# Performance work log

Measured on AMD Instinct MI355X. Metric: run time of the kernel, lower is better.

The kernel has to match this reference:

```python
import jax, jax.numpy as jnp
import numpy as np

N_HEADS = 8
D_K = 256
SCALE = D_K ** -0.5


def setup_inputs() -> dict:
    key = jax.random.key(0)
    k1, k2, k3 = jax.random.split(key, 3)
    B, C, H, W = 8, 256, 32, 32
    x = jax.random.normal(k1, (B, C, H, W), dtype=jnp.float32)
    Wp = jax.random.normal(k2, (C, N_HEADS * D_K * 3), dtype=jnp.float32) * (C ** -0.5)
    bp = jnp.zeros((N_HEADS * D_K * 3,), dtype=jnp.float32)
    Wo = jax.random.normal(k3, (N_HEADS * D_K, C), dtype=jnp.float32) * ((N_HEADS * D_K) ** -0.5)
    bo = jnp.zeros((C,), dtype=jnp.float32)
    return {"x": x, "Wp": Wp, "bp": bp, "Wo": Wo, "bo": bo}


def reference(x, Wp, bp, Wo, bo):
    B, C, H, W = x.shape
    S = H * W
    # [B,C,H,W] -> [B,S,C] tokens
    xt = x.reshape(B, C, S).transpose(0, 2, 1)
    qkv = (xt @ Wp + bp).reshape(B, S, N_HEADS, 3 * D_K)
    q, k, v = jnp.split(qkv, 3, axis=-1)  # each [B,S,H,dk]
    attn = jnp.einsum('bihd,bjhd->bijh', q, k) * SCALE
    attn = jax.nn.softmax(attn, axis=2)  # over j (keys)
    res = jnp.einsum('bijh,bjhd->bihd', attn, v).reshape(B, S, N_HEADS * D_K)
    res = res @ Wo + bo + xt  # residual
    return res.transpose(0, 2, 1).reshape(B, C, H, W)
```

## Files before the change

kernel.cpp:

```cpp
#include <hip/hip_runtime.h>

#define NH    8
#define DK    256
#define SS    1024
#define QSCALE 0.09016844136947155f

using frag8  = __attribute__((ext_vector_type(8))) short;
using f32x4  = __attribute__((ext_vector_type(4))) float;
using f32x16 = __attribute__((ext_vector_type(16))) float;

__device__ __forceinline__ unsigned short f2bf(float f) {
    unsigned int u = __float_as_uint(f);
    return (unsigned short)((u + 0x7FFFu + ((u >> 16) & 1u)) >> 16);
}

__device__ __forceinline__ void load_lds16(const void* g, void* l) {
    __builtin_amdgcn_global_load_lds(
        (const __attribute__((address_space(1))) unsigned int*)g,
        (__attribute__((address_space(3))) unsigned int*)l, 16, 0, 0);
}

__global__ __launch_bounds__(256) void k0_t(const float* __restrict__ in,
                                            unsigned short* __restrict__ out,
                                            int R, int C)
{
    __shared__ float tile[32][33];
    const int bz = blockIdx.z;
    const int c0 = blockIdx.x * 32, r0 = blockIdx.y * 32;
    const int tx = threadIdx.x & 31, ty = threadIdx.x >> 5;
    const float* ip = in + (size_t)bz * R * C;
    unsigned short* op = out + (size_t)bz * R * C;
#pragma unroll
    for (int j = 0; j < 4; j++)
        tile[ty + j * 8][tx] = ip[(size_t)(r0 + ty + j * 8) * C + c0 + tx];
    __syncthreads();
#pragma unroll
    for (int j = 0; j < 4; j++)
        op[(size_t)(c0 + ty + j * 8) * R + r0 + tx] = f2bf(tile[tx][ty + j * 8]);
}

__global__ __launch_bounds__(256) void k1_qkv(
    const unsigned short* __restrict__ xb, const unsigned short* __restrict__ Wpt,
    const float* __restrict__ bp,
    unsigned short* __restrict__ qb, unsigned short* __restrict__ kb,
    unsigned short* __restrict__ vb)
{
    __shared__ unsigned short As[128 * 32];
    __shared__ unsigned short Bs[128 * 32];
    const int t = threadIdx.x;
    const int wave = t >> 6, lane = t & 63;
    const int quad = lane >> 4, l16 = lane & 15;
    const int n0 = blockIdx.x * 128, m0 = blockIdx.y * 128;
    const int b = m0 >> 10, s0 = m0 & 1023;
    const int mq = (wave >> 1) * 64, nq = (wave & 1) * 64;
    const int lr = lane >> 2, lc = (lane & 3) * 8;

    const unsigned short* Ag = xb + (size_t)(b * 1024 + s0) * 256;
    const unsigned short* Bg = Wpt + (size_t)n0 * 256;

    f32x4 acc[4][4];
#pragma unroll
    for (int i = 0; i < 4; i++)
#pragma unroll
        for (int j = 0; j < 4; j++) acc[i][j] = (f32x4){0.f, 0.f, 0.f, 0.f};

    for (int k0 = 0; k0 < 256; k0 += 32) {
#pragma unroll
        for (int j = 0; j < 2; j++) {
            int ch = wave + j * 4;
            load_lds16(Ag + (size_t)(ch * 16 + lr) * 256 + k0 + lc, &As[ch * 512]);
            load_lds16(Bg + (size_t)(ch * 16 + lr) * 256 + k0 + lc, &Bs[ch * 512]);
        }
        __syncthreads();
        frag8 af[4], bf[4];
#pragma unroll
        for (int i = 0; i < 4; i++)
            af[i] = *(const frag8*)(&As[(mq + i * 16 + l16) * 32 + quad * 8]);
#pragma unroll
        for (int j = 0; j < 4; j++)
            bf[j] = *(const frag8*)(&Bs[(nq + j * 16 + l16) * 32 + quad * 8]);
#pragma unroll
        for (int i = 0; i < 4; i++)
#pragma unroll
            for (int j = 0; j < 4; j++)
                acc[i][j] = __builtin_amdgcn_mfma_f32_16x16x32_bf16(af[i], bf[j], acc[i][j], 0, 0, 0);
        __syncthreads();
    }

    const int h = n0 / 768;
    const int rem = n0 - h * 768;
    const int tt = rem >> 8;
    const int dbase = (rem & 255) + nq;
    const size_t bh = (size_t)(b * NH + h);
    float bias[4];
#pragma unroll
    for (int j = 0; j < 4; j++) bias[j] = bp[n0 + nq + j * 16 + l16];

    if (tt < 2) {
        const float sc = (tt == 0) ? QSCALE : 1.0f;
        unsigned short* dst = (tt == 0 ? qb : kb) + bh * SS * DK;
#pragma unroll
        for (int i = 0; i < 4; i++)
#pragma unroll
            for (int r = 0; r < 4; r++) {
                int s = s0 + mq + i * 16 + quad * 4 + r;
#pragma unroll
                for (int j = 0; j < 4; j++)
                    dst[(size_t)s * DK + dbase + j * 16 + l16] = f2bf((acc[i][j][r] + bias[j]) * sc);
            }
    } else {
        unsigned short* dst = vb + bh * DK * SS;
#pragma unroll
        for (int j = 0; j < 4; j++) {
            int d = dbase + j * 16 + l16;
#pragma unroll
            for (int i = 0; i < 4; i++)
#pragma unroll
                for (int r = 0; r < 4; r++)
                    dst[(size_t)d * SS + s0 + mq + i * 16 + quad * 4 + r]
                        = f2bf(acc[i][j][r] + bias[j]);
        }
    }
}

__global__ __launch_bounds__(256, 2) void k2_attn(
    const unsigned short* __restrict__ qb, const unsigned short* __restrict__ kb,
    const unsigned short* __restrict__ vb, unsigned short* __restrict__ ob)
{
    __shared__ unsigned short Ks[32 * 256];
    __shared__ unsigned short Vs[4 * 2048];
    __shared__ float Ls[4][32];

    const int t = threadIdx.x;
    const int wave = t >> 6, lane = t & 63;
    const int l32 = lane & 31, hw = lane >> 5;

    const int flat = blockIdx.x;
    const int xcd = flat & 7, tt2 = flat >> 3;
    const int qt = tt2 & 7;
    const int bh = xcd * 8 + (tt2 >> 3);

    const int qrow0 = qt * 128 + wave * 32;

    frag8 qf[16];
    {
        const unsigned short* qp = qb + ((size_t)bh * SS + qrow0 + l32) * DK + hw * 8;
#pragma unroll
        for (int s = 0; s < 16; s++) qf[s] = *(const frag8*)(qp + s * 16);
    }

    f32x16 acc[8];
#pragma unroll
    for (int nb = 0; nb < 8; nb++)
#pragma unroll
        for (int r = 0; r < 16; r++) acc[nb][r] = 0.f;
    float lsum = 0.f;

    const unsigned short* kstg = kb + ((size_t)bh * SS + (lane & 31)) * DK + (lane >> 5) * 8;
    const unsigned short* vstg = vb + (size_t)bh * DK * SS + (size_t)lane * SS;

    for (int kt = 0; kt < 32; kt++) {
#pragma unroll
        for (int jj = 0; jj < 4; jj++) {
            int i = wave * 4 + jj;
            load_lds16(kstg + (size_t)kt * 32 * DK + i * 16, &Ks[i * 512]);
            int kc = i & 3, dgrp = i >> 2;
            load_lds16(vstg + (size_t)dgrp * 64 * SS + kt * 32 + kc * 8,
                       &Vs[kc * 2048 + dgrp * 512]);
        }
        __syncthreads();

        f32x16 sa0, sa1;
#pragma unroll
        for (int r = 0; r < 16; r++) { sa0[r] = 0.f; sa1[r] = 0.f; }
#pragma unroll
        for (int s = 0; s < 16; s += 2) {
            frag8 kf0 = *(const frag8*)(&Ks[(2 * s + hw) * 256 + l32 * 8]);
            frag8 kf1 = *(const frag8*)(&Ks[(2 * s + 2 + hw) * 256 + l32 * 8]);
            sa0 = __builtin_amdgcn_mfma_f32_32x32x16_bf16(kf0, qf[s], sa0, 0, 0, 0);
            sa1 = __builtin_amdgcn_mfma_f32_32x32x16_bf16(kf1, qf[s + 1], sa1, 0, 0, 0);
        }

        frag8 pf[2];
#pragma unroll
        for (int half = 0; half < 2; half++) {
            float p[8], px[8];
#pragma unroll
            for (int e = 0; e < 8; e++) {
                p[e] = exp2f(sa0[half * 8 + e] + sa1[half * 8 + e]);
                lsum += p[e];
            }
#pragma unroll
            for (int e = 0; e < 8; e++) px[e] = __shfl_xor(p[e], 32);
            frag8 w;
#pragma unroll
            for (int j = 0; j < 4; j++) {
                w[j]     = (short)f2bf(hw ? px[4 + j] : p[j]);
                w[4 + j] = (short)f2bf(hw ? p[4 + j] : px[j]);
            }
            pf[half] = w;
        }

#pragma unroll
        for (int s01 = 0; s01 < 2; s01++)
#pragma unroll
            for (int nb = 0; nb < 8; nb++) {
                frag8 vf = *(const frag8*)(&Vs[(s01 * 2 + hw) * 2048 + (nb * 32 + l32) * 8]);
                acc[nb] = __builtin_amdgcn_mfma_f32_32x32x16_bf16(pf[s01], vf, acc[nb], 0, 0, 0);
            }
        __syncthreads();
    }

    lsum += __shfl_xor(lsum, 32);
    Ls[wave][l32] = 1.f / lsum;

    unsigned short* og = ob + ((size_t)bh * SS + qrow0) * DK + l32;
#pragma unroll
    for (int r = 0; r < 16; r++) {
        const int rowl = (r & 3) + 8 * (r >> 2) + 4 * hw;
        const float li = Ls[wave][rowl];
        unsigned short* orow = og + (size_t)rowl * DK;
#pragma unroll
        for (int nb = 0; nb < 8; nb++)
            orow[nb * 32] = f2bf(acc[nb][r] * li);
    }
}

__global__ __launch_bounds__(256) void k3_proj(
    const unsigned short* __restrict__ ob, const unsigned short* __restrict__ Wot,
    const float* __restrict__ bo, const float* __restrict__ x,
    float* __restrict__ out)
{
    __shared__ unsigned short As[64 * 32];
    __shared__ unsigned short Bs[64 * 32];
    const int t = threadIdx.x;
    const int wave = t >> 6, lane = t & 63;
    const int quad = lane >> 4, l16 = lane & 15;
    const int n0 = blockIdx.x * 64, m0 = blockIdx.y * 64;
    const int b = m0 >> 10, s0 = m0 & 1023;
    const int mq = (wave >> 1) * 32, nq = (wave & 1) * 32;
    const int lr = lane >> 2, lc = (lane & 3) * 8;

    const unsigned short* Bg = Wot + (size_t)n0 * 2048;

    f32x4 acc[2][2];
#pragma unroll
    for (int i = 0; i < 2; i++)
#pragma unroll
        for (int j = 0; j < 2; j++) acc[i][j] = (f32x4){0.f, 0.f, 0.f, 0.f};

    for (int k0 = 0; k0 < 2048; k0 += 32) {
        const int h = k0 >> 8, d0 = k0 & 255;
        const unsigned short* Ag = ob + (size_t)((b * 8 + h) * 1024 + s0) * 256 + d0;
        load_lds16(Ag + (size_t)(wave * 16 + lr) * 256 + lc, &As[wave * 512]);
        load_lds16(Bg + (size_t)(wave * 16 + lr) * 2048 + k0 + lc, &Bs[wave * 512]);
        __syncthreads();
        frag8 af[2], bf[2];
#pragma unroll
        for (int i = 0; i < 2; i++)
            af[i] = *(const frag8*)(&As[(mq + i * 16 + l16) * 32 + quad * 8]);
#pragma unroll
        for (int j = 0; j < 2; j++)
            bf[j] = *(const frag8*)(&Bs[(nq + j * 16 + l16) * 32 + quad * 8]);
#pragma unroll
        for (int i = 0; i < 2; i++)
#pragma unroll
            for (int j = 0; j < 2; j++)
                acc[i][j] = __builtin_amdgcn_mfma_f32_16x16x32_bf16(af[i], bf[j], acc[i][j], 0, 0, 0);
        __syncthreads();
    }

#pragma unroll
    for (int j = 0; j < 2; j++) {
        int c = n0 + nq + j * 16 + l16;
        float bias = bo[c];
#pragma unroll
        for (int i = 0; i < 2; i++) {
            int s = s0 + mq + i * 16 + quad * 4;
            size_t off = (size_t)(b * 256 + c) * 1024 + s;
            float4 xv = *(const float4*)(&x[off]);
            float4 ov;
            ov.x = acc[i][j][0] + bias + xv.x;
            ov.y = acc[i][j][1] + bias + xv.y;
            ov.z = acc[i][j][2] + bias + xv.z;
            ov.w = acc[i][j][3] + bias + xv.w;
            *(float4*)(&out[off]) = ov;
        }
    }
}

extern "C" void kernel_launch(void* const* d_in, const int* in_sizes, int n_in,
                              void* d_out, int out_size, void* d_ws, size_t ws_size,
                              hipStream_t stream)
{
    const float* x  = (const float*)d_in[0];
    const float* Wp = (const float*)d_in[1];
    const float* bp = (const float*)d_in[2];
    const float* Wo = (const float*)d_in[3];
    const float* bo = (const float*)d_in[4];
    float* out = (float*)d_out;

    char* ws = (char*)d_ws;
    unsigned short* qb  = (unsigned short*)(ws);
    unsigned short* kb  = (unsigned short*)(ws + 33554432);
    unsigned short* vb  = (unsigned short*)(ws + 67108864);
    unsigned short* xb  = (unsigned short*)(ws + 100663296);
    unsigned short* Wpt = (unsigned short*)(ws + 104857600);
    unsigned short* Wot = (unsigned short*)(ws + 108003328);

    k0_t<<<dim3(32, 8, 8), 256, 0, stream>>>(x, xb, 256, 1024);
    k0_t<<<dim3(192, 8, 1), 256, 0, stream>>>(Wp, Wpt, 256, 6144);
    k0_t<<<dim3(8, 64, 1), 256, 0, stream>>>(Wo, Wot, 2048, 256);
    k1_qkv<<<dim3(48, 64), 256, 0, stream>>>(xb, Wpt, bp, qb, kb, vb);
    k2_attn<<<dim3(512), 256, 0, stream>>>(qb, kb, vb, qb );
    k3_proj<<<dim3(4, 128), 256, 0, stream>>>(qb, Wot, bo, x, out);
}
```

Before: 257.8 us.

## Tile Q/K/V into LDS-contiguous layout and double-buffer K/V loads in attention

```diff
diff --git a/kernel.cpp b/kernel.cpp
--- a/kernel.cpp
+++ b/kernel.cpp
@@ -4,6 +4,7 @@
 #define DK    256
 #define SS    1024
 #define QSCALE 0.09016844136947155f
+#define TSH   8192
 
 using frag8  = __attribute__((ext_vector_type(8))) short;
 using f32x4  = __attribute__((ext_vector_type(4))) float;
@@ -19,6 +20,7 @@
         (const __attribute__((address_space(1))) unsigned int*)g,
         (__attribute__((address_space(3))) unsigned int*)l, 16, 0, 0);
 }
+
 
 __global__ __launch_bounds__(256) void k0_t(const float* __restrict__ in,
                                             unsigned short* __restrict__ out,
@@ -98,27 +100,32 @@
 
     if (tt < 2) {
         const float sc = (tt == 0) ? QSCALE : 1.0f;
-        unsigned short* dst = (tt == 0 ? qb : kb) + bh * SS * DK;
+        unsigned short* dst = (tt == 0 ? qb : kb) + bh * 32 * TSH;
 #pragma unroll
         for (int i = 0; i < 4; i++)
 #pragma unroll
             for (int r = 0; r < 4; r++) {
                 int s = s0 + mq + i * 16 + quad * 4 + r;
-#pragma unroll
-                for (int j = 0; j < 4; j++)
-                    dst[(size_t)s * DK + dbase + j * 16 + l16] = f2bf((acc[i][j][r] + bias[j]) * sc);
+                const size_t tb = (size_t)(s >> 5) * TSH + (s & 31) * 8;
+#pragma unroll
+                for (int j = 0; j < 4; j++) {
+                    int d = dbase + j * 16 + l16;
+                    dst[tb + (d >> 3) * 256 + (d & 7)] = f2bf((acc[i][j][r] + bias[j]) * sc);
+                }
             }
     } else {
-        unsigned short* dst = vb + bh * DK * SS;
+        unsigned short* dst = vb + bh * 32 * TSH;
 #pragma unroll
         for (int j = 0; j < 4; j++) {
             int d = dbase + j * 16 + l16;
 #pragma unroll
             for (int i = 0; i < 4; i++)
 #pragma unroll
-                for (int r = 0; r < 4; r++)
-                    dst[(size_t)d * SS + s0 + mq + i * 16 + quad * 4 + r]
+                for (int r = 0; r < 4; r++) {
+                    int s = s0 + mq + i * 16 + quad * 4 + r;
+                    dst[(size_t)(s >> 5) * TSH + ((s >> 3) & 3) * 2048 + d * 8 + (s & 7)]
                         = f2bf(acc[i][j][r] + bias[j]);
+                }
         }
     }
 }
@@ -127,9 +134,8 @@
     const unsigned short* __restrict__ qb, const unsigned short* __restrict__ kb,
     const unsigned short* __restrict__ vb, unsigned short* __restrict__ ob)
 {
-    __shared__ unsigned short Ks[32 * 256];
-    __shared__ unsigned short Vs[4 * 2048];
-    __shared__ float Ls[4][32];
+    __shared__ unsigned short Ks[2][TSH];
+    __shared__ unsigned short Vs[2][TSH];
 
     const int t = threadIdx.x;
     const int wave = t >> 6, lane = t & 63;
@@ -144,9 +150,10 @@
 
     frag8 qf[16];
     {
-        const unsigned short* qp = qb + ((size_t)bh * SS + qrow0 + l32) * DK + hw * 8;
-#pragma unroll
-        for (int s = 0; s < 16; s++) qf[s] = *(const frag8*)(qp + s * 16);
+        const unsigned short* qp = qb + ((size_t)bh * 32 + qt * 4 + wave) * TSH
+                                 + hw * 256 + l32 * 8;
+#pragma unroll
+        for (int s = 0; s < 16; s++) qf[s] = *(const frag8*)(qp + s * 512);
     }
 
     f32x16 acc[8];
@@ -156,27 +163,38 @@
         for (int r = 0; r < 16; r++) acc[nb][r] = 0.f;
     float lsum = 0.f;
 
-    const unsigned short* kstg = kb + ((size_t)bh * SS + (lane & 31)) * DK + (lane >> 5) * 8;
-    const unsigned short* vstg = vb + (size_t)bh * DK * SS + (size_t)lane * SS;
+    const unsigned short* kt0 = kb + (size_t)bh * 32 * TSH;
+    const unsigned short* vt0 = vb + (size_t)bh * 32 * TSH;
+
+#pragma unroll
+    for (int j = 0; j < 4; j++) {
+        int c = wave * 4 + j;
+        load_lds16(kt0 + c * 512 + lane * 8, &Ks[0][c * 512]);
+        load_lds16(vt0 + c * 512 + lane * 8, &Vs[0][c * 512]);
+    }
+    __syncthreads();
 
     for (int kt = 0; kt < 32; kt++) {
-#pragma unroll
-        for (int jj = 0; jj < 4; jj++) {
-            int i = wave * 4 + jj;
-            load_lds16(kstg + (size_t)kt * 32 * DK + i * 16, &Ks[i * 512]);
-            int kc = i & 3, dgrp = i >> 2;
-            load_lds16(vstg + (size_t)dgrp * 64 * SS + kt * 32 + kc * 8,
-                       &Vs[kc * 2048 + dgrp * 512]);
-        }
-        __syncthreads();
+        const int cur = kt & 1;
+
+        if (kt < 31) {
+            const unsigned short* kg = kt0 + (size_t)(kt + 1) * TSH;
+            const unsigned short* vg = vt0 + (size_t)(kt + 1) * TSH;
+#pragma unroll
+            for (int j = 0; j < 4; j++) {
+                int c = wave * 4 + j;
+                load_lds16(kg + c * 512 + lane * 8, &Ks[cur ^ 1][c * 512]);
+                load_lds16(vg + c * 512 + lane * 8, &Vs[cur ^ 1][c * 512]);
+            }
+        }
 
         f32x16 sa0, sa1;
 #pragma unroll
         for (int r = 0; r < 16; r++) { sa0[r] = 0.f; sa1[r] = 0.f; }
 #pragma unroll
         for (int s = 0; s < 16; s += 2) {
-            frag8 kf0 = *(const frag8*)(&Ks[(2 * s + hw) * 256 + l32 * 8]);
-            frag8 kf1 = *(const frag8*)(&Ks[(2 * s + 2 + hw) * 256 + l32 * 8]);
+            frag8 kf0 = *(const frag8*)(&Ks[cur][(2 * s + hw) * 256 + l32 * 8]);
+            frag8 kf1 = *(const frag8*)(&Ks[cur][(2 * s + 2 + hw) * 256 + l32 * 8]);
             sa0 = __builtin_amdgcn_mfma_f32_32x32x16_bf16(kf0, qf[s], sa0, 0, 0, 0);
             sa1 = __builtin_amdgcn_mfma_f32_32x32x16_bf16(kf1, qf[s + 1], sa1, 0, 0, 0);
         }
@@ -205,20 +223,21 @@
         for (int s01 = 0; s01 < 2; s01++)
 #pragma unroll
             for (int nb = 0; nb < 8; nb++) {
-                frag8 vf = *(const frag8*)(&Vs[(s01 * 2 + hw) * 2048 + (nb * 32 + l32) * 8]);
+                frag8 vf = *(const frag8*)(&Vs[cur][(s01 * 2 + hw) * 2048 + (nb * 32 + l32) * 8]);
                 acc[nb] = __builtin_amdgcn_mfma_f32_32x32x16_bf16(pf[s01], vf, acc[nb], 0, 0, 0);
             }
+
         __syncthreads();
     }
 
     lsum += __shfl_xor(lsum, 32);
-    Ls[wave][l32] = 1.f / lsum;
+    const float linv = 1.f / lsum;
 
     unsigned short* og = ob + ((size_t)bh * SS + qrow0) * DK + l32;
 #pragma unroll
     for (int r = 0; r < 16; r++) {
         const int rowl = (r & 3) + 8 * (r >> 2) + 4 * hw;
-        const float li = Ls[wave][rowl];
+        const float li = __shfl(linv, rowl, 64);
         unsigned short* orow = og + (size_t)rowl * DK;
 #pragma unroll
         for (int nb = 0; nb < 8; nb++)
```

Result: faster. 233.9 us (-9.3%).
